# Kernel optimization log

Hardware: AMD Instinct MI355X
Metric: run time of the kernel (lower is better)

Reference implementation:

```python
import jax, jax.numpy as jnp
import numpy as np

T_LEN, E_LEN, BATCH, DIM = 32, 256, 16, 512  # topic_len, exp_len, batch, input=hidden size
HID = 512


def setup_inputs() -> dict:
    key = jax.random.key(0)
    k1, k2, k3, k4, k5, k6 = jax.random.split(key, 6)
    topic = jax.random.normal(k1, (T_LEN, BATCH, DIM), dtype=jnp.float32)
    exp_output = jax.random.normal(k2, (E_LEN, BATCH, DIM), dtype=jnp.float32)
    seq_mask = jax.random.bernoulli(k3, 0.1, (E_LEN, BATCH))  # True = masked exp position
    # nn.Linear(hidden+input, hidden): weight [HID, HID+DIM], bias [HID]
    lim1 = 1.0 / np.sqrt(HID + DIM)
    W_attn = jax.random.uniform(k4, (HID, HID + DIM), minval=-lim1, maxval=lim1, dtype=jnp.float32)
    b_attn = jax.random.uniform(k5, (HID,), minval=-lim1, maxval=lim1, dtype=jnp.float32)
    # nn.Linear(hidden, 1): weight [1, HID], bias [1]
    lim2 = 1.0 / np.sqrt(HID)
    kv, kb = jax.random.split(k6)
    v_score = jax.random.uniform(kv, (1, HID), minval=-lim2, maxval=lim2, dtype=jnp.float32)
    b_score = jax.random.uniform(kb, (1,), minval=-lim2, maxval=lim2, dtype=jnp.float32)
    return {"topic": topic, "exp_output": exp_output, "seq_mask": seq_mask,
            "W_attn": W_attn, "b_attn": b_attn, "v_score": v_score, "b_score": b_score}


def reference(topic, exp_output, seq_mask, W_attn, b_attn, v_score, b_score):
    # topic: [T, B, D]; exp_output: [E, B, D]; seq_mask: [E, B] bool
    D = topic.shape[2]
    # Split the concat-Linear: cat(topic, exp) @ W.T == topic @ W[:, :D].T + exp @ W[:, D:].T
    proj_t = jnp.einsum('tbd,hd->bth', topic, W_attn[:, :D])        # [B, T, H]
    proj_e = jnp.einsum('ebd,hd->beh', exp_output, W_attn[:, D:])   # [B, E, H]
    feat = jnp.tanh(proj_t[:, :, None, :] + proj_e[:, None, :, :] + b_attn)  # [B, T, E, H]
    energies = jnp.einsum('bteh,h->bte', feat, v_score[0]) + b_score[0]      # [B, T, E]
    # mask exp positions (broadcast over topic dim), as masked_fill(-1e12)
    energies = jnp.where(seq_mask.T[:, None, :], jnp.float32(-1e12), energies)
    attn_s1 = jax.nn.softmax(jnp.swapaxes(energies, 1, 2), axis=2)  # [B, E, T], softmax over topics
    attn_s2 = jax.nn.softmax(energies, axis=2)                      # [B, T, E], softmax over exp
    new_exp = jnp.einsum('bet,btd->bed', attn_s1, jnp.swapaxes(topic, 0, 1))       # [B, E, D]
    new_topic = jnp.einsum('bte,bed->btd', attn_s2, jnp.swapaxes(exp_output, 0, 1))  # [B, T, D]
    return new_topic, new_exp
```

## Files before the change

### kernel.cpp

```cpp
#include <hip/hip_runtime.h>
#include <hip/hip_bf16.h>
#include <cstddef>
#include <cstdint>

#define T_LEN 32
#define E_LEN 256
#define BATCH 16
#define DIM 512
#define HID 512
#define WROW 1024

#define TWO_LOG2E 2.8853900817779268f

typedef __attribute__((ext_vector_type(8))) short bf16x8;
typedef __attribute__((ext_vector_type(4))) float f32x4;

__device__ inline bf16x8 cvt8(float4 a, float4 b) {
    union { bf16x8 v; __hip_bfloat16 h[8]; } u;
    u.h[0] = __float2bfloat16(a.x); u.h[1] = __float2bfloat16(a.y);
    u.h[2] = __float2bfloat16(a.z); u.h[3] = __float2bfloat16(a.w);
    u.h[4] = __float2bfloat16(b.x); u.h[5] = __float2bfloat16(b.y);
    u.h[6] = __float2bfloat16(b.z); u.h[7] = __float2bfloat16(b.w);
    return u.v;
}

#define GPAD 8
#define GLDR (64 + GPAD)

__global__ __launch_bounds__(256) void gemm_fused(
    const float* __restrict__ topic, const float* __restrict__ expo,
    const float* __restrict__ W, const float* __restrict__ battn,
    float* __restrict__ EPT, float* __restrict__ EPE) {
    __shared__ __hip_bfloat16 As[64 * GLDR];
    __shared__ __hip_bfloat16 Bs[64 * GLDR];
    const int tid = threadIdx.x;
    const int by = blockIdx.y;
    const float* A; const float* Wp; const float* bias; float* C; int m0;
    if (by < 8) { A = topic; Wp = W;       bias = battn;   C = EPT; m0 = by * 64; }
    else        { A = expo;  Wp = W + DIM; bias = nullptr; C = EPE; m0 = (by - 8) * 64; }
    const int n0 = blockIdx.x * 64;
    const int w = tid >> 6;
    const int lane = tid & 63;
    const int l15 = lane & 15;
    const int g = lane >> 4;
    const int srow = tid >> 2;
    const int sc = tid & 3;

    f32x4 acc[4];
    const f32x4 z = {0.f, 0.f, 0.f, 0.f};
#pragma unroll
    for (int nt = 0; nt < 4; ++nt) acc[nt] = z;

    const float* ga = A + (size_t)(m0 + srow) * 512 + sc * 8;
    const float* gb = Wp + (size_t)(n0 + srow) * WROW + sc * 8;

    float4 a0 = *(const float4*)(ga);
    float4 a1 = *(const float4*)(ga + 4);
    float4 a2 = *(const float4*)(ga + 32);
    float4 a3 = *(const float4*)(ga + 36);
    float4 b0 = *(const float4*)(gb);
    float4 b1 = *(const float4*)(gb + 4);
    float4 b2 = *(const float4*)(gb + 32);
    float4 b3 = *(const float4*)(gb + 36);

    for (int kk = 0; kk < 8; ++kk) {
        bf16x8 av0 = cvt8(a0, a1), av1 = cvt8(a2, a3);
        bf16x8 bv0 = cvt8(b0, b1), bv1 = cvt8(b2, b3);
        if (kk < 7) {
            ga += 64; gb += 64;
            a0 = *(const float4*)(ga);
            a1 = *(const float4*)(ga + 4);
            a2 = *(const float4*)(ga + 32);
            a3 = *(const float4*)(ga + 36);
            b0 = *(const float4*)(gb);
            b1 = *(const float4*)(gb + 4);
            b2 = *(const float4*)(gb + 32);
            b3 = *(const float4*)(gb + 36);
        }
        __syncthreads();
        *(bf16x8*)&As[srow * GLDR + sc * 8] = av0;
        *(bf16x8*)&As[srow * GLDR + sc * 8 + 32] = av1;
        *(bf16x8*)&Bs[srow * GLDR + sc * 8] = bv0;
        *(bf16x8*)&Bs[srow * GLDR + sc * 8 + 32] = bv1;
        __syncthreads();
#pragma unroll
        for (int s = 0; s < 2; ++s) {
            bf16x8 af = *(const bf16x8*)&As[(w * 16 + l15) * GLDR + (s * 4 + g) * 8];
#pragma unroll
            for (int nt = 0; nt < 4; ++nt) {
                bf16x8 bf = *(const bf16x8*)&Bs[(nt * 16 + l15) * GLDR + (s * 4 + g) * 8];
                acc[nt] = __builtin_amdgcn_mfma_f32_16x16x32_bf16(af, bf, acc[nt], 0, 0, 0);
            }
        }
    }
#pragma unroll
    for (int nt = 0; nt < 4; ++nt) {
        int n = n0 + nt * 16 + l15;
        float bv = bias ? bias[n] : 0.f;
#pragma unroll
        for (int r = 0; r < 4; ++r) {
            int m = m0 + w * 16 + g * 4 + r;
            C[(size_t)m * 512 + n] = __builtin_amdgcn_exp2f((acc[nt][r] + bv) * TWO_LOG2E);
        }
    }
}

__global__ __launch_bounds__(256) void energies_k(const float* __restrict__ EPT,
                                                  const float* __restrict__ EPE,
                                                  const float* __restrict__ v,
                                                  const float* __restrict__ bscore,
                                                  const int* __restrict__ mask,
                                                  float* __restrict__ EN) {
    const int b = blockIdx.x;
    const int tg = blockIdx.y;
    const int ech = blockIdx.z;
    const int lane = threadIdx.x & 63;
    const int w = threadIdx.x >> 6;
    const int h0 = lane * 8;
    const int e0 = ech * 16 + w * 4;

    int mk[4];
#pragma unroll
    for (int ei = 0; ei < 4; ++ei) mk[ei] = mask[(e0 + ei) * BATCH + b];

    float sv[8], spt[4][8];
    float sumv;
    {
        float4 v0 = *(const float4*)(v + h0);
        float4 v1 = *(const float4*)(v + h0 + 4);
        float vr[8] = {v0.x, v0.y, v0.z, v0.w, v1.x, v1.y, v1.z, v1.w};
        float s = 0.f;
#pragma unroll
        for (int j = 0; j < 8; ++j) { sv[j] = -2.f * vr[j]; s += vr[j]; }
#pragma unroll
        for (int off = 32; off; off >>= 1) s += __shfl_xor(s, off);
        sumv = s;
#pragma unroll
        for (int i = 0; i < 4; ++i) {
            const float* p = EPT + ((size_t)((tg * 4 + i) * BATCH + b)) * HID + h0;
            float4 p0 = *(const float4*)(p);
            float4 p1 = *(const float4*)(p + 4);
            spt[i][0] = p0.x; spt[i][1] = p0.y; spt[i][2] = p0.z; spt[i][3] = p0.w;
            spt[i][4] = p1.x; spt[i][5] = p1.y; spt[i][6] = p1.z; spt[i][7] = p1.w;
        }
    }
    const float bs = bscore[0];
#pragma unroll
    for (int ei = 0; ei < 4; ++ei) {
        const int e = e0 + ei;
        if (mk[ei] != 0) {
            if (lane == 0) {
#pragma unroll
                for (int i = 0; i < 4; ++i)
                    EN[((size_t)b * T_LEN + tg * 4 + i) * E_LEN + e] = -1e12f;
            }
            continue;
        }
        const float* pe = EPE + ((size_t)(e * BATCH + b)) * HID + h0;
        float4 p0 = *(const float4*)(pe);
        float4 p1 = *(const float4*)(pe + 4);
        float pr[8] = {p0.x, p0.y, p0.z, p0.w, p1.x, p1.y, p1.z, p1.w};
        float acc[4] = {0.f, 0.f, 0.f, 0.f};
#pragma unroll
        for (int i = 0; i < 4; ++i) {
#pragma unroll
            for (int j = 0; j < 8; ++j) {
                float q = fmaf(spt[i][j], pr[j], 1.0f);
                float r = __builtin_amdgcn_rcpf(q);
                acc[i] = fmaf(sv[j], r, acc[i]);
            }
        }
#pragma unroll
        for (int i = 0; i < 4; ++i) {
#pragma unroll
            for (int off = 32; off; off >>= 1) acc[i] += __shfl_xor(acc[i], off);
        }
        if (lane == 0) {
#pragma unroll
            for (int i = 0; i < 4; ++i) {
                EN[((size_t)b * T_LEN + tg * 4 + i) * E_LEN + e] = sumv + bs + acc[i];
            }
        }
    }
}

__global__ __launch_bounds__(256) void epilogue_k(const float* __restrict__ EN,
                                                  const float* __restrict__ topic,
                                                  const float* __restrict__ expo,
                                                  float* __restrict__ out) {
    __shared__ float smem[2560];
    const int tid = threadIdx.x;
    const int lane = tid & 63;
    const int w = tid >> 6;
    if (blockIdx.x < 512) {
        const int b = blockIdx.x >> 5;
        const int ech = (blockIdx.x >> 1) & 15;
        const int hf = blockIdx.x & 1;
        const int e0 = ech * 16 + w * 4;
        float wv[4];
#pragma unroll
        for (int ei = 0; ei < 4; ++ei) {
            const int e = e0 + ei;
            float x = (lane < T_LEN) ? EN[((size_t)b * T_LEN + lane) * E_LEN + e] : -3e38f;
            float m = x;
#pragma unroll
            for (int off = 16; off; off >>= 1) m = fmaxf(m, __shfl_xor(m, off));
            float p = (lane < T_LEN) ? __expf(x - m) : 0.f;
            float s = p;
#pragma unroll
            for (int off = 16; off; off >>= 1) s += __shfl_xor(s, off);
            wv[ei] = __fdividef(p, s);
        }
        const int d0 = hf * 256 + lane * 4;
        float4 acc[4];
#pragma unroll
        for (int ei = 0; ei < 4; ++ei) acc[ei] = {0.f, 0.f, 0.f, 0.f};
        for (int t = 0; t < T_LEN; ++t) {
            float4 r = *(const float4*)(topic + ((size_t)t * BATCH + b) * DIM + d0);
            float wt[4];
#pragma unroll
            for (int ei = 0; ei < 4; ++ei) wt[ei] = __shfl(wv[ei], t);
#pragma unroll
            for (int ei = 0; ei < 4; ++ei) {
                acc[ei].x = fmaf(wt[ei], r.x, acc[ei].x);
                acc[ei].y = fmaf(wt[ei], r.y, acc[ei].y);
                acc[ei].z = fmaf(wt[ei], r.z, acc[ei].z);
                acc[ei].w = fmaf(wt[ei], r.w, acc[ei].w);
            }
        }
#pragma unroll
        for (int ei = 0; ei < 4; ++ei) {
            float* o = out + (size_t)BATCH * T_LEN * DIM +
                       ((size_t)b * E_LEN + e0 + ei) * DIM + d0;
            *(float4*)o = acc[ei];
        }
    } else {
        const int q = blockIdx.x - 512;
        const int b = q >> 5;
        const int tp = (q >> 1) & 15;
        const int hf = q & 1;
        if (w < 2) {
            const int bt = b * T_LEN + tp * 2 + w;
            float4 xv = *(const float4*)&EN[(size_t)bt * E_LEN + lane * 4];
            float m = fmaxf(fmaxf(xv.x, xv.y), fmaxf(xv.z, xv.w));
#pragma unroll
            for (int off = 32; off; off >>= 1) m = fmaxf(m, __shfl_xor(m, off));
            float p0 = __expf(xv.x - m), p1 = __expf(xv.y - m);
            float p2 = __expf(xv.z - m), p3 = __expf(xv.w - m);
            float s = p0 + p1 + p2 + p3;
#pragma unroll
            for (int off = 32; off; off >>= 1) s += __shfl_xor(s, off);
            float inv = __fdividef(1.f, s);
            float4 wvv = {p0 * inv, p1 * inv, p2 * inv, p3 * inv};
            *(float4*)&smem[w * 256 + lane * 4] = wvv;
        }
        __syncthreads();
        const int dl = lane * 4;
        const int dglob = hf * 256 + dl;
        float4 a0 = {0.f, 0.f, 0.f, 0.f};
        float4 a1 = {0.f, 0.f, 0.f, 0.f};
        const float* base = expo + (size_t)b * DIM + dglob;
        for (int ee = 0; ee < 64; ++ee) {
            const int e = w * 64 + ee;
            float4 rv = *(const float4*)(base + (size_t)e * BATCH * DIM);
            float w0 = smem[e];
            float w1 = smem[256 + e];
            a0.x = fmaf(w0, rv.x, a0.x); a0.y = fmaf(w0, rv.y, a0.y);
            a0.z = fmaf(w0, rv.z, a0.z); a0.w = fmaf(w0, rv.w, a0.w);
            a1.x = fmaf(w1, rv.x, a1.x); a1.y = fmaf(w1, rv.y, a1.y);
            a1.z = fmaf(w1, rv.z, a1.z); a1.w = fmaf(w1, rv.w, a1.w);
        }
        *(float4*)&smem[512 + (w * 2 + 0) * 256 + dl] = a0;
        *(float4*)&smem[512 + (w * 2 + 1) * 256 + dl] = a1;
        __syncthreads();
#pragma unroll
        for (int tt = 0; tt < 2; ++tt) {
            float sum = smem[512 + (0 * 2 + tt) * 256 + tid] +
                        smem[512 + (1 * 2 + tt) * 256 + tid] +
                        smem[512 + (2 * 2 + tt) * 256 + tid] +
                        smem[512 + (3 * 2 + tt) * 256 + tid];
            out[((size_t)b * T_LEN + tp * 2 + tt) * DIM + hf * 256 + tid] = sum;
        }
    }
}

extern "C" void kernel_launch(void* const* d_in, const int* in_sizes, int n_in,
                              void* d_out, int out_size, void* d_ws, size_t ws_size,
                              hipStream_t stream) {
    const float* topic = (const float*)d_in[0];
    const float* expo  = (const float*)d_in[1];
    const int*   mask  = (const int*)d_in[2];
    const float* W     = (const float*)d_in[3];
    const float* battn = (const float*)d_in[4];
    const float* vsc   = (const float*)d_in[5];
    const float* bsc   = (const float*)d_in[6];
    float* out = (float*)d_out;

    float* EPT = (float*)d_ws;
    float* EPE = EPT + (size_t)T_LEN * BATCH * HID;
    float* EN  = EPE + (size_t)E_LEN * BATCH * HID;

    gemm_fused<<<dim3(8, 72), 256, 0, stream>>>(topic, expo, W, battn, EPT, EPE);
    energies_k<<<dim3(BATCH, 8, 16), 256, 0, stream>>>(EPT, EPE, vsc, bsc, mask, EN);
    epilogue_k<<<1024, 256, 0, stream>>>(EN, topic, expo, out);
}
```

Before: 115.4 us.

## Emit unnormalized exp energies and drop max-subtraction from softmaxes

```diff
diff --git a/kernel.cpp b/kernel.cpp
--- a/kernel.cpp
+++ b/kernel.cpp
@@ -11,6 +11,7 @@
 #define WROW 1024
 
 #define TWO_LOG2E 2.8853900817779268f
+#define LOG2E 1.4426950408889634f
 
 typedef __attribute__((ext_vector_type(8))) short bf16x8;
 typedef __attribute__((ext_vector_type(4))) float f32x4;
@@ -108,9 +109,8 @@
 __global__ __launch_bounds__(256) void energies_k(const float* __restrict__ EPT,
                                                   const float* __restrict__ EPE,
                                                   const float* __restrict__ v,
-                                                  const float* __restrict__ bscore,
                                                   const int* __restrict__ mask,
-                                                  float* __restrict__ EN) {
+                                                  float* __restrict__ P) {
     const int b = blockIdx.x;
     const int tg = blockIdx.y;
     const int ech = blockIdx.z;
@@ -123,68 +123,63 @@
 #pragma unroll
     for (int ei = 0; ei < 4; ++ei) mk[ei] = mask[(e0 + ei) * BATCH + b];
 
-    float sv[8], spt[4][8];
-    float sumv;
+    float sv[8], spt[8][8];
     {
         float4 v0 = *(const float4*)(v + h0);
         float4 v1 = *(const float4*)(v + h0 + 4);
-        float vr[8] = {v0.x, v0.y, v0.z, v0.w, v1.x, v1.y, v1.z, v1.w};
-        float s = 0.f;
-#pragma unroll
-        for (int j = 0; j < 8; ++j) { sv[j] = -2.f * vr[j]; s += vr[j]; }
-#pragma unroll
-        for (int off = 32; off; off >>= 1) s += __shfl_xor(s, off);
-        sumv = s;
-#pragma unroll
-        for (int i = 0; i < 4; ++i) {
-            const float* p = EPT + ((size_t)((tg * 4 + i) * BATCH + b)) * HID + h0;
+        sv[0] = -2.f * v0.x; sv[1] = -2.f * v0.y; sv[2] = -2.f * v0.z; sv[3] = -2.f * v0.w;
+        sv[4] = -2.f * v1.x; sv[5] = -2.f * v1.y; sv[6] = -2.f * v1.z; sv[7] = -2.f * v1.w;
+#pragma unroll
+        for (int i = 0; i < 8; ++i) {
+            const float* p = EPT + ((size_t)((tg * 8 + i) * BATCH + b)) * HID + h0;
             float4 p0 = *(const float4*)(p);
             float4 p1 = *(const float4*)(p + 4);
             spt[i][0] = p0.x; spt[i][1] = p0.y; spt[i][2] = p0.z; spt[i][3] = p0.w;
             spt[i][4] = p1.x; spt[i][5] = p1.y; spt[i][6] = p1.z; spt[i][7] = p1.w;
         }
     }
-    const float bs = bscore[0];
 #pragma unroll
     for (int ei = 0; ei < 4; ++ei) {
         const int e = e0 + ei;
         if (mk[ei] != 0) {
-            if (lane == 0) {
-#pragma unroll
-                for (int i = 0; i < 4; ++i)
-                    EN[((size_t)b * T_LEN + tg * 4 + i) * E_LEN + e] = -1e12f;
-            }
+            if (lane < 8)
+                P[((size_t)b * T_LEN + tg * 8 + lane) * E_LEN + e] = 1e-30f;
             continue;
         }
         const float* pe = EPE + ((size_t)(e * BATCH + b)) * HID + h0;
         float4 p0 = *(const float4*)(pe);
         float4 p1 = *(const float4*)(pe + 4);
         float pr[8] = {p0.x, p0.y, p0.z, p0.w, p1.x, p1.y, p1.z, p1.w};
-        float acc[4] = {0.f, 0.f, 0.f, 0.f};
-#pragma unroll
-        for (int i = 0; i < 4; ++i) {
+        float a[8] = {0.f, 0.f, 0.f, 0.f, 0.f, 0.f, 0.f, 0.f};
+#pragma unroll
+        for (int i = 0; i < 8; ++i) {
 #pragma unroll
             for (int j = 0; j < 8; ++j) {
                 float q = fmaf(spt[i][j], pr[j], 1.0f);
                 float r = __builtin_amdgcn_rcpf(q);
-                acc[i] = fmaf(sv[j], r, acc[i]);
+                a[i] = fmaf(sv[j], r, a[i]);
             }
         }
 #pragma unroll
-        for (int i = 0; i < 4; ++i) {
-#pragma unroll
-            for (int off = 32; off; off >>= 1) acc[i] += __shfl_xor(acc[i], off);
-        }
-        if (lane == 0) {
-#pragma unroll
-            for (int i = 0; i < 4; ++i) {
-                EN[((size_t)b * T_LEN + tg * 4 + i) * E_LEN + e] = sumv + bs + acc[i];
-            }
-        }
-    }
-}
-
-__global__ __launch_bounds__(256) void epilogue_k(const float* __restrict__ EN,
+        for (int i = 0; i < 8; ++i) {
+            a[i] += __shfl_xor(a[i], 1);
+            a[i] += __shfl_xor(a[i], 2);
+            a[i] += __shfl_xor(a[i], 4);
+            a[i] += __shfl_xor(a[i], 8);
+        }
+        const int sel = lane & 3;
+        float uA = sel == 0 ? a[0] : sel == 1 ? a[1] : sel == 2 ? a[2] : a[3];
+        float uB = sel == 0 ? a[4] : sel == 1 ? a[5] : sel == 2 ? a[6] : a[7];
+        uA += __shfl_xor(uA, 16); uA += __shfl_xor(uA, 32);
+        uB += __shfl_xor(uB, 16); uB += __shfl_xor(uB, 32);
+        float u = (lane & 4) ? uB : uA;
+        if (lane < 8)
+            P[((size_t)b * T_LEN + tg * 8 + lane) * E_LEN + e] =
+                __builtin_amdgcn_exp2f(u * LOG2E);
+    }
+}
+
+__global__ __launch_bounds__(256) void epilogue_k(const float* __restrict__ P,
                                                   const float* __restrict__ topic,
                                                   const float* __restrict__ expo,
                                                   float* __restrict__ out) {
@@ -201,15 +196,11 @@
 #pragma unroll
         for (int ei = 0; ei < 4; ++ei) {
             const int e = e0 + ei;
-            float x = (lane < T_LEN) ? EN[((size_t)b * T_LEN + lane) * E_LEN + e] : -3e38f;
-            float m = x;
-#pragma unroll
-            for (int off = 16; off; off >>= 1) m = fmaxf(m, __shfl_xor(m, off));
-            float p = (lane < T_LEN) ? __expf(x - m) : 0.f;
-            float s = p;
-#pragma unroll
-            for (int off = 16; off; off >>= 1) s += __shfl_xor(s, off);
-            wv[ei] = __fdividef(p, s);
+            float x = (lane < T_LEN) ? P[((size_t)b * T_LEN + lane) * E_LEN + e] : 0.f;
+            float s = x;
+#pragma unroll
+            for (int off = 32; off; off >>= 1) s += __shfl_xor(s, off);
+            wv[ei] = x * __builtin_amdgcn_rcpf(s);
         }
         const int d0 = hf * 256 + lane * 4;
         float4 acc[4];
@@ -241,17 +232,12 @@
         const int hf = q & 1;
         if (w < 2) {
             const int bt = b * T_LEN + tp * 2 + w;
-            float4 xv = *(const float4*)&EN[(size_t)bt * E_LEN + lane * 4];
-            float m = fmaxf(fmaxf(xv.x, xv.y), fmaxf(xv.z, xv.w));
-#pragma unroll
-            for (int off = 32; off; off >>= 1) m = fmaxf(m, __shfl_xor(m, off));
-            float p0 = __expf(xv.x - m), p1 = __expf(xv.y - m);
-            float p2 = __expf(xv.z - m), p3 = __expf(xv.w - m);
-            float s = p0 + p1 + p2 + p3;
+            float4 xv = *(const float4*)&P[(size_t)bt * E_LEN + lane * 4];
+            float s = xv.x + xv.y + xv.z + xv.w;
 #pragma unroll
             for (int off = 32; off; off >>= 1) s += __shfl_xor(s, off);
-            float inv = __fdividef(1.f, s);
-            float4 wvv = {p0 * inv, p1 * inv, p2 * inv, p3 * inv};
+            float inv = __builtin_amdgcn_rcpf(s);
+            float4 wvv = {xv.x * inv, xv.y * inv, xv.z * inv, xv.w * inv};
             *(float4*)&smem[w * 256 + lane * 4] = wvv;
         }
         __syncthreads();
@@ -293,14 +279,13 @@
     const float* W     = (const float*)d_in[3];
     const float* battn = (const float*)d_in[4];
     const float* vsc   = (const float*)d_in[5];
-    const float* bsc   = (const float*)d_in[6];
     float* out = (float*)d_out;
 
     float* EPT = (float*)d_ws;
     float* EPE = EPT + (size_t)T_LEN * BATCH * HID;
-    float* EN  = EPE + (size_t)E_LEN * BATCH * HID;
+    float* P   = EPE + (size_t)E_LEN * BATCH * HID;
 
     gemm_fused<<<dim3(8, 72), 256, 0, stream>>>(topic, expo, W, battn, EPT, EPE);
-    energies_k<<<dim3(BATCH, 8, 16), 256, 0, stream>>>(EPT, EPE, vsc, bsc, mask, EN);
-    epilogue_k<<<1024, 256, 0, stream>>>(EN, topic, expo, out);
-}
+    energies_k<<<dim3(BATCH, 4, 16), 256, 0, stream>>>(EPT, EPE, vsc, mask, P);
+    epilogue_k<<<1024, 256, 0, stream>>>(P, topic, expo, out);
+}
```

Measured after the change: 114.5 us. No clear change (-0.8%).
